# Kernel tuning notes

Hardware: AMD Instinct MI355X
Metric: run time of the kernel (lower is better)

The kernel has to match this reference:

```python
import jax, jax.numpy as jnp
import numpy as np

B, C, H, W = 8, 256, 64, 64
HEADS, H_SP, W_SP = 8, 64, 4  # idx=0: H_sp=resolution[0], W_sp=split_size
D = C // HEADS
SCALE = D ** -0.5
HH, WW = H // H_SP, W // W_SP  # 1, 16 (no padding needed)


def setup_inputs() -> dict:
    key = jax.random.key(0)
    k1, k2, k3 = jax.random.split(key, 3)
    temp = jax.random.normal(k1, (B, 3, C, H, W), dtype=jnp.float32)
    get_v_weight = jax.random.normal(k2, (C, 1, 3, 3), dtype=jnp.float32) * 0.1
    get_v_bias = jax.random.normal(k3, (C,), dtype=jnp.float32) * 0.1
    return {"temp": temp, "get_v_weight": get_v_weight, "get_v_bias": get_v_bias}


def _im2win_shuffle(x):
    # x: (B, C, H, W); H split as (H_SP, HH) with H_SP OUTER (shuffled windows)
    x = x.reshape(B, HEADS, D, H_SP, HH, W_SP, WW)
    x = x.transpose(0, 4, 6, 1, 3, 5, 2)  # b hh ww h H_sp W_sp d
    return x.reshape(B * HH * WW, HEADS, H_SP * W_SP, D)


def reference(temp, get_v_weight, get_v_bias):
    # H, W are multiples of H_SP, W_SP -> pad is zero (faithful to F.pad path)
    q, k, v = temp[:, 0], temp[:, 1], temp[:, 2]
    qw = _im2win_shuffle(q) * SCALE
    kw = _im2win_shuffle(k)
    vw = _im2win_shuffle(v)

    # LePE: depthwise 3x3 conv applied per shuffled window
    vimg = v.reshape(B, C, H_SP, HH, W_SP, WW).transpose(0, 3, 5, 1, 2, 4)
    vimg = vimg.reshape(B * HH * WW, C, H_SP, W_SP)
    lepe = jax.lax.conv_general_dilated(
        vimg, get_v_weight, (1, 1), ((1, 1), (1, 1)),
        dimension_numbers=("NCHW", "OIHW", "NCHW"), feature_group_count=C,
    ) + get_v_bias[None, :, None, None]
    lepe = lepe.reshape(B * HH * WW, HEADS, D, H_SP * W_SP).transpose(0, 1, 3, 2)

    attn = jax.nn.softmax(jnp.einsum("whqd,whkd->whqk", qw, kw), axis=-1)
    x = jnp.einsum("whqk,whkd->whqd", attn, vw) + lepe  # (nW, h, S, d)

    # windows2img_shuffle -> (B, C, H, W), then raw .view to (B, H, W, C)
    x = x.reshape(B, HH, WW, HEADS, H_SP, W_SP, D)
    x = x.transpose(0, 3, 6, 4, 1, 5, 2).reshape(B, C, H, W)
    x = x.reshape(B, H, W, C)  # raw memory view, matches torch .view
    return x.reshape(B, H * W, C)
```

## Files before the change

### kernel.cpp

```cpp
#include <hip/hip_runtime.h>


typedef __attribute__((ext_vector_type(8))) short bf16x8;
typedef __attribute__((ext_vector_type(4))) float floatx4;
typedef unsigned short ushort_t;
typedef unsigned int uint_t;

constexpr float QSCALE = 0.25503486f;

__device__ __forceinline__ ushort_t f2bf(float f) {
    union { float f; uint_t u; } v; v.f = f;
    uint_t r = v.u + 0x7fffu + ((v.u >> 16) & 1u);
    return (ushort_t)(r >> 16);
}
__device__ __forceinline__ float bf2f(ushort_t h) {
    union { uint_t u; float f; } v; v.u = ((uint_t)h) << 16;
    return v.f;
}
__device__ __forceinline__ float bfu2f(uint_t bits) {
    union { uint_t u; float f; } v; v.u = bits; return v.f;
}
__device__ __forceinline__ uint_t cvtpk(float lo, float hi) {
    uint_t r;
    asm("v_cvt_pk_bf16_f32 %0, %1, %2" : "=v"(r) : "v"(lo), "v"(hi));
    return r;
}

constexpr int KP    = 1280;
constexpr int VBASE = 4 * KP;
constexpr int VP    = 1280;
constexpr int SMU   = VBASE + 4 * VP;
constexpr int LDP   = 74;
constexpr int LPS   = 32 * LDP;
constexpr int OPS   = 530;

__global__ __launch_bounds__(256, 6)
void fused_kernel(const float* __restrict__ temp, const float* __restrict__ wgt,
                  const float* __restrict__ bias, float* __restrict__ out)
{
    const int bid = blockIdx.x;
    const int hd = bid & 7;
    const int b  = (bid >> 3) & 7;
    const int wq = (bid >> 6) & 3;
    const int qq = bid >> 8;

    __shared__ __align__(16) ushort_t SM[SMU];

    const int u = threadIdx.x;
    const int w = u >> 6;
    const int ln = u & 63;
    const int lm = ln & 15, q4 = ln >> 4;

    const float4* Tq4 = (const float4*)temp + ((size_t)((b * 3 + 0) * 256 + hd * 32)) * 1024 + wq;
    const float4* Tk4 = Tq4 + (size_t)256 * 1024;
    const float4* Tv4 = Tk4 + (size_t)256 * 1024;

    union F4 { float4 v; float a[4]; };

    bf16x8 qa[4];
    #pragma unroll
    for (int pass = 0; pass < 4; pass++) {
        {
            const int tq = u & 15, d2 = u >> 4;
            const int d = d2 * 2;
            const int tg = qq * 64 + pass * 16 + tq;
            F4 v0, v1;
            v0.v = Tq4[(size_t)d * 1024 + tg * 4];
            v1.v = Tq4[(size_t)(d + 1) * 1024 + tg * 4];
            #pragma unroll
            for (int j = 0; j < 4; j++)
                *(uint_t*)&SM[j * KP + tq * 40 + d] =
                    cvtpk(v0.a[j] * QSCALE, v1.a[j] * QSCALE);
        }
        __syncthreads();
        qa[pass] = *(const bf16x8*)&SM[w * KP + lm * 40 + q4 * 8];
        __syncthreads();
    }

    floatx4 acc[4][2];
    float lsum[4];
    #pragma unroll
    for (int T = 0; T < 4; T++) {
        acc[T][0] = (floatx4)0.0f; acc[T][1] = (floatx4)0.0f;
        lsum[T] = 0.0f;
    }

    const int k0row = ((lm >> 2) << 3) + (lm & 3);
    const int pKb = w * KP;
    const int pVb = VBASE + w * VP;

    for (int kt = 0; kt < 8; kt++) {
        #pragma unroll
        for (int i = 0; i < 2; i++) {
            const int flat = i * 256 + u;
            const int k = flat & 31, d2 = flat >> 5;
            const int d = d2 * 2;
            F4 v0, v1;
            v0.v = Tk4[(size_t)d * 1024 + (kt * 32 + k) * 4];
            v1.v = Tk4[(size_t)(d + 1) * 1024 + (kt * 32 + k) * 4];
            #pragma unroll
            for (int j = 0; j < 4; j++)
                *(uint_t*)&SM[j * KP + k * 40 + d] = cvtpk(v0.a[j], v1.a[j]);
        }
        #pragma unroll
        for (int i = 0; i < 2; i++) {
            const int flat = i * 256 + u;
            const int k2 = flat & 15, dv = flat >> 4;
            F4 va, vb;
            va.v = Tv4[(size_t)dv * 1024 + (kt * 32 + k2 * 2) * 4];
            vb.v = Tv4[(size_t)dv * 1024 + (kt * 32 + k2 * 2 + 1) * 4];
            #pragma unroll
            for (int j = 0; j < 4; j++)
                *(uint_t*)&SM[VBASE + j * VP + dv * 40 + k2 * 2] = cvtpk(va.a[j], vb.a[j]);
        }
        __syncthreads();

        const bf16x8 kb0 = *(const bf16x8*)&SM[pKb + k0row * 40 + q4 * 8];
        const bf16x8 kb1 = *(const bf16x8*)&SM[pKb + (k0row + 4) * 40 + q4 * 8];
        const bf16x8 vb0 = *(const bf16x8*)&SM[pVb + lm * 40 + q4 * 8];
        const bf16x8 vb1 = *(const bf16x8*)&SM[pVb + (16 + lm) * 40 + q4 * 8];
        #pragma unroll
        for (int T = 0; T < 4; T++) {
            floatx4 s0 = __builtin_amdgcn_mfma_f32_16x16x32_bf16(kb0, qa[T], (floatx4)0.0f, 0, 0, 0);
            floatx4 s1 = __builtin_amdgcn_mfma_f32_16x16x32_bf16(kb1, qa[T], (floatx4)0.0f, 0, 0, 0);
            const uint_t u0 = cvtpk(exp2f(s0[0]), exp2f(s0[1]));
            const uint_t u1 = cvtpk(exp2f(s0[2]), exp2f(s0[3]));
            const uint_t u2 = cvtpk(exp2f(s1[0]), exp2f(s1[1]));
            const uint_t u3 = cvtpk(exp2f(s1[2]), exp2f(s1[3]));
            lsum[T] += bfu2f(u0 << 16) + bfu2f(u0 & 0xffff0000u)
                     + bfu2f(u1 << 16) + bfu2f(u1 & 0xffff0000u)
                     + bfu2f(u2 << 16) + bfu2f(u2 & 0xffff0000u)
                     + bfu2f(u3 << 16) + bfu2f(u3 & 0xffff0000u);
            union { uint_t pw[4]; bf16x8 v; } pa;
            pa.pw[0] = u0; pa.pw[1] = u1; pa.pw[2] = u2; pa.pw[3] = u3;
            acc[T][0] = __builtin_amdgcn_mfma_f32_16x16x32_bf16(pa.v, vb0, acc[T][0], 0, 0, 0);
            acc[T][1] = __builtin_amdgcn_mfma_f32_16x16x32_bf16(pa.v, vb1, acc[T][1], 0, 0, 0);
        }
        __syncthreads();
    }

    #pragma unroll
    for (int i = 0; i < 9; i++) {
        const int flat = i * 256 + u;
        const int wsp = flat & 3;
        const int rem = flat >> 2;
        const int d = rem / 18, hl = rem - d * 18;
        const int hh = qq * 16 - 1 + hl;
        F4 v;
        if ((unsigned)hh < 64u) v.v = Tv4[(size_t)d * 1024 + hh * 16 + wsp * 4];
        else { v.a[0] = 0.f; v.a[1] = 0.f; v.a[2] = 0.f; v.a[3] = 0.f; }
        #pragma unroll
        for (int j = 0; j < 4; j++)
            SM[j * LPS + d * LDP + hl * 4 + wsp] = f2bf(v.a[j]);
    }
    __syncthreads();

    float wc[2][9], bs2[2];
    #pragma unroll
    for (int dt = 0; dt < 2; dt++) {
        const int d = dt * 16 + lm;
        #pragma unroll
        for (int k = 0; k < 9; k++) wc[dt][k] = wgt[(hd * 32 + d) * 9 + k];
        bs2[dt] = bias[hd * 32 + d];
    }

    #pragma unroll
    for (int T = 0; T < 4; T++) {
        float tot = lsum[T];
        tot += __shfl_xor(tot, 16);
        tot += __shfl_xor(tot, 32);
        float inv[4];
        #pragma unroll
        for (int r = 0; r < 4; r++) inv[r] = 1.0f / __shfl(tot, q4 * 4 + r);

        #pragma unroll
        for (int dt = 0; dt < 2; dt++) {
            const int d = dt * 16 + lm;
            float vv[3][4];
            #pragma unroll
            for (int dy = 0; dy < 3; dy++) {
                const int hl = T * 4 + q4 + dy;
                #pragma unroll
                for (int cx = 0; cx < 4; cx++)
                    vv[dy][cx] = bf2f(SM[w * LPS + d * LDP + hl * 4 + cx]);
            }
            #pragma unroll
            for (int r = 0; r < 4; r++) {
                float lep = bs2[dt];
                #pragma unroll
                for (int dy = 0; dy < 3; dy++) {
                    #pragma unroll
                    for (int kx = 0; kx < 3; kx++) {
                        const int wsrc = r + kx - 1;
                        if (wsrc >= 0 && wsrc < 4) lep += wc[dt][dy * 3 + kx] * vv[dy][wsrc];
                    }
                }
                acc[T][dt][r] = acc[T][dt][r] * inv[r] + lep;
            }
        }
    }
    __syncthreads();

    float* Ob = (float*)SM;
    float4* out4 = (float4*)out + ((size_t)(b * 256 + hd * 32)) * 1024 + wq;
    #pragma unroll
    for (int T = 0; T < 4; T++) {
        #pragma unroll
        for (int dt = 0; dt < 2; dt++) {
            #pragma unroll
            for (int r = 0; r < 4; r++)
                Ob[w * OPS + (q4 * 4 + r) * 33 + dt * 16 + lm] = acc[T][dt][r];
        }
        __syncthreads();
        #pragma unroll
        for (int i = 0; i < 2; i++) {
            const int flat = i * 256 + u;
            const int q = flat & 15, d = flat >> 4;
            float4 o;
            o.x = Ob[0 * OPS + q * 33 + d];
            o.y = Ob[1 * OPS + q * 33 + d];
            o.z = Ob[2 * OPS + q * 33 + d];
            o.w = Ob[3 * OPS + q * 33 + d];
            out4[(size_t)d * 1024 + (qq * 64 + T * 16 + q) * 4] = o;
        }
        __syncthreads();
    }
}

extern "C" void kernel_launch(void* const* d_in, const int* in_sizes, int n_in,
                              void* d_out, int out_size, void* d_ws, size_t ws_size,
                              hipStream_t stream) {
    const float* temp = (const float*)d_in[0];
    const float* wgt  = (const float*)d_in[1];
    const float* bias = (const float*)d_in[2];
    float* out = (float*)d_out;
    (void)d_ws; (void)ws_size;
    fused_kernel<<<dim3(1024), dim3(256), 0, stream>>>(temp, wgt, bias, out);
}
```

Measured before the change: 245.9 us.

## Merge four window blocks into 1024-thread blocks with double-buffered K/V prefetch

Each block now covers all four width-windows of a head and query tile, so 16 waves share one block. Global loads of Q/K/V and the output stores become contiguous float4 accesses across the windows. The K/V loop gains double-buffered LDS with a register prefetch two chunks ahead, which halves the barriers per step and overlaps loads with MFMA work. In exchange the block uses about 147KB of LDS, so each CU holds a single block. The launch bound asking for four 1024-thread blocks per CU may also force a very low VGPR cap and cause spills.

```diff
diff --git a/kernel.cpp b/kernel.cpp
--- a/kernel.cpp
+++ b/kernel.cpp
@@ -26,23 +26,25 @@
     return r;
 }
 
-constexpr int KP    = 1280;
-constexpr int VBASE = 4 * KP;
-constexpr int VP    = 1280;
-constexpr int SMU   = VBASE + 4 * VP;
+constexpr int KPP   = 1280;
+constexpr int KBUFS = 16 * KPP;
+constexpr int VBASE = 2 * KBUFS;
+constexpr int VPP   = 1024;
+constexpr int VBUFS = 16 * VPP;
+constexpr int SMU   = VBASE + 2 * VBUFS;
+constexpr int QPP   = 2560;
 constexpr int LDP   = 74;
 constexpr int LPS   = 32 * LDP;
 constexpr int OPS   = 530;
 
-__global__ __launch_bounds__(256, 6)
+__global__ __launch_bounds__(1024, 4)
 void fused_kernel(const float* __restrict__ temp, const float* __restrict__ wgt,
                   const float* __restrict__ bias, float* __restrict__ out)
 {
     const int bid = blockIdx.x;
     const int hd = bid & 7;
     const int b  = (bid >> 3) & 7;
-    const int wq = (bid >> 6) & 3;
-    const int qq = bid >> 8;
+    const int qq = bid >> 6;
 
     __shared__ __align__(16) ushort_t SM[SMU];
 
@@ -51,31 +53,58 @@
     const int ln = u & 63;
     const int lm = ln & 15, q4 = ln >> 4;
 
-    const float4* Tq4 = (const float4*)temp + ((size_t)((b * 3 + 0) * 256 + hd * 32)) * 1024 + wq;
+    const float4* Tq4 = (const float4*)temp + ((size_t)((b * 3 + 0) * 256 + hd * 32)) * 1024;
     const float4* Tk4 = Tq4 + (size_t)256 * 1024;
     const float4* Tv4 = Tk4 + (size_t)256 * 1024;
 
     union F4 { float4 v; float a[4]; };
 
+    #pragma unroll
+    for (int i = 0; i < 4; i++) {
+        const int flat = i * 1024 + u;
+        const int tq = flat & 63, wwg = (flat >> 6) & 3, d2 = flat >> 8;
+        F4 v0, v1;
+        v0.v = Tq4[(size_t)(2 * d2) * 1024 + (qq * 64 + tq) * 4 + wwg];
+        v1.v = Tq4[(size_t)(2 * d2 + 1) * 1024 + (qq * 64 + tq) * 4 + wwg];
+        #pragma unroll
+        for (int j = 0; j < 4; j++)
+            *(uint_t*)&SM[(wwg * 4 + j) * QPP + tq * 40 + d2 * 2] =
+                cvtpk(v0.a[j] * QSCALE, v1.a[j] * QSCALE);
+    }
+    __syncthreads();
     bf16x8 qa[4];
     #pragma unroll
-    for (int pass = 0; pass < 4; pass++) {
-        {
-            const int tq = u & 15, d2 = u >> 4;
-            const int d = d2 * 2;
-            const int tg = qq * 64 + pass * 16 + tq;
-            F4 v0, v1;
-            v0.v = Tq4[(size_t)d * 1024 + tg * 4];
-            v1.v = Tq4[(size_t)(d + 1) * 1024 + tg * 4];
-            #pragma unroll
-            for (int j = 0; j < 4; j++)
-                *(uint_t*)&SM[j * KP + tq * 40 + d] =
-                    cvtpk(v0.a[j] * QSCALE, v1.a[j] * QSCALE);
-        }
-        __syncthreads();
-        qa[pass] = *(const bf16x8*)&SM[w * KP + lm * 40 + q4 * 8];
-        __syncthreads();
-    }
+    for (int T = 0; T < 4; T++)
+        qa[T] = *(const bf16x8*)&SM[w * QPP + (T * 16 + lm) * 40 + q4 * 8];
+    __syncthreads();
+
+    const int kk = u & 31, kwg = (u >> 5) & 3, kd2 = u >> 7;
+    const int vk2 = u & 15, vwg = (u >> 4) & 3, vd = u >> 6;
+
+    F4 k0a, k0b, k1a, k1b, w0a, w0b, w1a, w1b;
+
+#define LOADC(cc) do { const int bt = (cc) * 32;                               \
+    k0a.v = Tk4[(size_t)(2 * kd2) * 1024      + (bt + kk) * 4 + kwg];          \
+    k0b.v = Tk4[(size_t)(2 * kd2 + 1) * 1024  + (bt + kk) * 4 + kwg];          \
+    k1a.v = Tk4[(size_t)(2 * kd2 + 16) * 1024 + (bt + kk) * 4 + kwg];          \
+    k1b.v = Tk4[(size_t)(2 * kd2 + 17) * 1024 + (bt + kk) * 4 + kwg];          \
+    w0a.v = Tv4[(size_t)vd * 1024        + (bt + 2 * vk2) * 4 + vwg];          \
+    w0b.v = Tv4[(size_t)vd * 1024        + (bt + 2 * vk2 + 1) * 4 + vwg];      \
+    w1a.v = Tv4[(size_t)(vd + 16) * 1024 + (bt + 2 * vk2) * 4 + vwg];          \
+    w1b.v = Tv4[(size_t)(vd + 16) * 1024 + (bt + 2 * vk2 + 1) * 4 + vwg];      \
+  } while (0)
+
+#define COMMITC(bf) do {                                                                        \
+    _Pragma("unroll")                                                                           \
+    for (int j = 0; j < 4; j++) {                                                               \
+        *(uint_t*)&SM[(bf) * KBUFS + (kwg * 4 + j) * KPP + kk * 40 + kd2 * 2]       = cvtpk(k0a.a[j], k0b.a[j]); \
+        *(uint_t*)&SM[(bf) * KBUFS + (kwg * 4 + j) * KPP + kk * 40 + (kd2 + 8) * 2] = cvtpk(k1a.a[j], k1b.a[j]); \
+        *(uint_t*)&SM[VBASE + (bf) * VBUFS + (vwg * 4 + j) * VPP + vd * 32 + vk2 * 2]        = cvtpk(w0a.a[j], w0b.a[j]); \
+        *(uint_t*)&SM[VBASE + (bf) * VBUFS + (vwg * 4 + j) * VPP + (vd + 16) * 32 + vk2 * 2] = cvtpk(w1a.a[j], w1b.a[j]); \
+    } } while (0)
+
+    LOADC(0); COMMITC(0); LOADC(1);
+    __syncthreads();
 
     floatx4 acc[4][2];
     float lsum[4];
@@ -84,41 +113,16 @@
         acc[T][0] = (floatx4)0.0f; acc[T][1] = (floatx4)0.0f;
         lsum[T] = 0.0f;
     }
-
     const int k0row = ((lm >> 2) << 3) + (lm & 3);
-    const int pKb = w * KP;
-    const int pVb = VBASE + w * VP;
-
-    for (int kt = 0; kt < 8; kt++) {
-        #pragma unroll
-        for (int i = 0; i < 2; i++) {
-            const int flat = i * 256 + u;
-            const int k = flat & 31, d2 = flat >> 5;
-            const int d = d2 * 2;
-            F4 v0, v1;
-            v0.v = Tk4[(size_t)d * 1024 + (kt * 32 + k) * 4];
-            v1.v = Tk4[(size_t)(d + 1) * 1024 + (kt * 32 + k) * 4];
-            #pragma unroll
-            for (int j = 0; j < 4; j++)
-                *(uint_t*)&SM[j * KP + k * 40 + d] = cvtpk(v0.a[j], v1.a[j]);
-        }
-        #pragma unroll
-        for (int i = 0; i < 2; i++) {
-            const int flat = i * 256 + u;
-            const int k2 = flat & 15, dv = flat >> 4;
-            F4 va, vb;
-            va.v = Tv4[(size_t)dv * 1024 + (kt * 32 + k2 * 2) * 4];
-            vb.v = Tv4[(size_t)dv * 1024 + (kt * 32 + k2 * 2 + 1) * 4];
-            #pragma unroll
-            for (int j = 0; j < 4; j++)
-                *(uint_t*)&SM[VBASE + j * VP + dv * 40 + k2 * 2] = cvtpk(va.a[j], vb.a[j]);
-        }
-        __syncthreads();
-
-        const bf16x8 kb0 = *(const bf16x8*)&SM[pKb + k0row * 40 + q4 * 8];
-        const bf16x8 kb1 = *(const bf16x8*)&SM[pKb + (k0row + 4) * 40 + q4 * 8];
-        const bf16x8 vb0 = *(const bf16x8*)&SM[pVb + lm * 40 + q4 * 8];
-        const bf16x8 vb1 = *(const bf16x8*)&SM[pVb + (16 + lm) * 40 + q4 * 8];
+
+    #pragma unroll 2
+    for (int c = 0; c < 8; c++) {
+        const int bK = (c & 1) * KBUFS + w * KPP;
+        const int bV = VBASE + (c & 1) * VBUFS + w * VPP;
+        const bf16x8 kb0 = *(const bf16x8*)&SM[bK + k0row * 40 + q4 * 8];
+        const bf16x8 kb1 = *(const bf16x8*)&SM[bK + (k0row + 4) * 40 + q4 * 8];
+        const bf16x8 vb0 = *(const bf16x8*)&SM[bV + lm * 32 + q4 * 8];
+        const bf16x8 vb1 = *(const bf16x8*)&SM[bV + (16 + lm) * 32 + q4 * 8];
         #pragma unroll
         for (int T = 0; T < 4; T++) {
             floatx4 s0 = __builtin_amdgcn_mfma_f32_16x16x32_bf16(kb0, qa[T], (floatx4)0.0f, 0, 0, 0);
@@ -136,22 +140,27 @@
             acc[T][0] = __builtin_amdgcn_mfma_f32_16x16x32_bf16(pa.v, vb0, acc[T][0], 0, 0, 0);
             acc[T][1] = __builtin_amdgcn_mfma_f32_16x16x32_bf16(pa.v, vb1, acc[T][1], 0, 0, 0);
         }
-        __syncthreads();
-    }
+        if (c < 7) {
+            COMMITC((c + 1) & 1);
+            if (c < 6) LOADC(c + 2);
+            __syncthreads();
+        }
+    }
+    __syncthreads();
 
     #pragma unroll
     for (int i = 0; i < 9; i++) {
-        const int flat = i * 256 + u;
-        const int wsp = flat & 3;
-        const int rem = flat >> 2;
+        const int flat = i * 1024 + u;
+        const int wsp = flat & 3, wwg = (flat >> 2) & 3;
+        const int rem = flat >> 4;
         const int d = rem / 18, hl = rem - d * 18;
         const int hh = qq * 16 - 1 + hl;
         F4 v;
-        if ((unsigned)hh < 64u) v.v = Tv4[(size_t)d * 1024 + hh * 16 + wsp * 4];
+        if ((unsigned)hh < 64u) v.v = Tv4[(size_t)d * 1024 + hh * 16 + wsp * 4 + wwg];
         else { v.a[0] = 0.f; v.a[1] = 0.f; v.a[2] = 0.f; v.a[3] = 0.f; }
         #pragma unroll
         for (int j = 0; j < 4; j++)
-            SM[j * LPS + d * LDP + hl * 4 + wsp] = f2bf(v.a[j]);
+            SM[(wwg * 4 + j) * LPS + d * LDP + hl * 4 + wsp] = f2bf(v.a[j]);
     }
     __syncthreads();
 
@@ -202,7 +211,7 @@
     __syncthreads();
 
     float* Ob = (float*)SM;
-    float4* out4 = (float4*)out + ((size_t)(b * 256 + hd * 32)) * 1024 + wq;
+    float4* out4 = (float4*)out + ((size_t)(b * 256 + hd * 32)) * 1024;
     #pragma unroll
     for (int T = 0; T < 4; T++) {
         #pragma unroll
@@ -214,17 +223,19 @@
         __syncthreads();
         #pragma unroll
         for (int i = 0; i < 2; i++) {
-            const int flat = i * 256 + u;
-            const int q = flat & 15, d = flat >> 4;
+            const int flat = i * 1024 + u;
+            const int q = flat & 15, wwg = (flat >> 4) & 3, d = flat >> 6;
             float4 o;
-            o.x = Ob[0 * OPS + q * 33 + d];
-            o.y = Ob[1 * OPS + q * 33 + d];
-            o.z = Ob[2 * OPS + q * 33 + d];
-            o.w = Ob[3 * OPS + q * 33 + d];
-            out4[(size_t)d * 1024 + (qq * 64 + T * 16 + q) * 4] = o;
+            o.x = Ob[(wwg * 4 + 0) * OPS + q * 33 + d];
+            o.y = Ob[(wwg * 4 + 1) * OPS + q * 33 + d];
+            o.z = Ob[(wwg * 4 + 2) * OPS + q * 33 + d];
+            o.w = Ob[(wwg * 4 + 3) * OPS + q * 33 + d];
+            out4[(size_t)d * 1024 + (qq * 64 + T * 16 + q) * 4 + wwg] = o;
         }
         __syncthreads();
     }
+#undef LOADC
+#undef COMMITC
 }
 
 extern "C" void kernel_launch(void* const* d_in, const int* in_sizes, int n_in,
@@ -235,5 +246,5 @@
     const float* bias = (const float*)d_in[2];
     float* out = (float*)d_out;
     (void)d_ws; (void)ws_size;
-    fused_kernel<<<dim3(1024), dim3(256), 0, stream>>>(temp, wgt, bias, out);
-}
+    fused_kernel<<<dim3(256), dim3(1024), 0, stream>>>(temp, wgt, bias, out);
+}
```

Result: faster. 232.9 us (-5.3%).
